# Kernel optimization log

Measured on AMD Instinct MI355X. Metric: run time of the kernel, lower is better.

The kernel has to match this reference:

```python
import jax, jax.numpy as jnp
import numpy as np

B, S, H, NH = 2, 2048, 1024, 16
HD = H // NH  # 64


def setup_inputs() -> dict:
    key = jax.random.key(0)
    ks = jax.random.split(key, 9)
    w = lambda k: jax.random.normal(k, (H, H), dtype=jnp.float32) * 0.02  # torch Linear weight [out,in]
    b = lambda k: jax.random.normal(k, (H,), dtype=jnp.float32) * 0.02
    return {
        "hidden_states": jax.random.normal(ks[0], (B, S, H), dtype=jnp.float32),
        "Wq": w(ks[1]), "bq": b(ks[2]),
        "Wk": w(ks[3]), "bk": b(ks[4]),
        "Wv": w(ks[5]), "bv": b(ks[6]),
        "Wo": w(ks[7]), "bo": b(ks[8]),
    }


def reference(hidden_states, Wq, bq, Wk, bk, Wv, bv, Wo, bo):
    b, s, h = hidden_states.shape
    nh, hd = NH, h // NH

    def proj(W, bias):
        y = hidden_states @ W.T + bias  # torch Linear: x W^T + b
        return y.reshape(b, s, nh, hd).transpose(0, 2, 1, 3)  # [b, h, s, d]

    q = proj(Wq, bq)
    k = proj(Wk, bk)
    v = proj(Wv, bv)

    scale = jnp.sqrt(jnp.asarray(hd, dtype=q.dtype))
    scores = jnp.einsum("bhqd,bhkd->bhqk", q, k) / scale  # [b, h, s, s]
    pos = jnp.arange(s)
    causal = pos[:, None] < pos[None, :]  # True where masked (key after query)
    scores = jnp.where(causal[None, None], -jnp.inf, scores)
    attn = jax.nn.softmax(scores, axis=-1)
    out = jnp.einsum("bhqk,bhkd->bhqd", attn, v)
    out = out.transpose(0, 2, 1, 3).reshape(b, s, h)
    return out @ Wo.T + bo
```

## Files before the change

kernel.cpp:

```cpp
#include <hip/hip_runtime.h>
#include <stdint.h>

typedef __bf16 bf16;
typedef __attribute__((ext_vector_type(2))) __bf16 bf16x2;
typedef __attribute__((ext_vector_type(4))) __bf16 bf16x4;
typedef __attribute__((ext_vector_type(8))) __bf16 bf16x8;
typedef __attribute__((ext_vector_type(4))) float f32x4;
typedef __attribute__((ext_vector_type(4))) short s16x4;

#define B_  2
#define S_  2048
#define H_  1024
#define NH_ 16
#define HD_ 64

__device__ __forceinline__ void glds16(const bf16* g, bf16* l) {
  __builtin_amdgcn_global_load_lds(
      (const __attribute__((address_space(1))) uint32_t*)g,
      (__attribute__((address_space(3))) uint32_t*)l, 16, 0, 0);
}

__device__ __forceinline__ f32x4 pv_mfma(bf16x4 a, bf16x4 b, f32x4 c) {
#if __has_builtin(__builtin_amdgcn_mfma_f32_16x16x16bf16_1k)
  union U { bf16x4 h; s16x4 s; };
  U ua; ua.h = a;
  U ub; ub.h = b;
  return __builtin_amdgcn_mfma_f32_16x16x16bf16_1k(ua.s, ub.s, c, 0, 0, 0);
#else
  f32x4 d;
  asm volatile("v_mfma_f32_16x16x16_bf16 %0, %1, %2, %3\n\ts_nop 7\n\ts_nop 7"
               : "=v"(d) : "v"(a), "v"(b), "v"(c));
  return d;
#endif
}

__device__ __forceinline__ void cvt16_store(const float4 v[4], bf16* dst) {
  bf16x8 o0, o1;
  o0[0] = (bf16)v[0].x; o0[1] = (bf16)v[0].y; o0[2] = (bf16)v[0].z; o0[3] = (bf16)v[0].w;
  o0[4] = (bf16)v[1].x; o0[5] = (bf16)v[1].y; o0[6] = (bf16)v[1].z; o0[7] = (bf16)v[1].w;
  o1[0] = (bf16)v[2].x; o1[1] = (bf16)v[2].y; o1[2] = (bf16)v[2].z; o1[3] = (bf16)v[2].w;
  o1[4] = (bf16)v[3].x; o1[5] = (bf16)v[3].y; o1[6] = (bf16)v[3].z; o1[7] = (bf16)v[3].w;
  *(bf16x8*)(dst)     = o0;
  *(bf16x8*)(dst + 8) = o1;
}

#define LD4(dst, src)                                                       \
  { dst[0] = *(const float4*)(src);      dst[1] = *(const float4*)((src) + 4); \
    dst[2] = *(const float4*)((src) + 8); dst[3] = *(const float4*)((src) + 12); }

__global__ __launch_bounds__(256) void gemm_qkv_f32(
    const float* __restrict__ X,
    const float* __restrict__ Wqf, const float* __restrict__ Wkf,
    const float* __restrict__ Wvf,
    const float* __restrict__ bq, const float* __restrict__ bk,
    const float* __restrict__ bv,
    bf16* __restrict__ Yq, bf16* __restrict__ Yk, bf16* __restrict__ Yv,
    float qscl)
{
  __shared__ __align__(16) bf16 As[2][128 * 32];
  __shared__ __align__(16) bf16 Bs[2][128 * 32];

  const int tid  = threadIdx.x;
  const int lane = tid & 63;
  const int wave = tid >> 6;

  const int m0  = blockIdx.y * 128;
  const int n0g = blockIdx.x * 128;
  const int seg = n0g >> 10;
  const float* W    = seg == 0 ? Wqf : (seg == 1 ? Wkf : Wvf);
  const float* bias = seg == 0 ? bq  : (seg == 1 ? bk  : bv);
  bf16*        Y    = seg == 0 ? Yq  : (seg == 1 ? Yk  : Yv);
  const float  ysc  = seg == 0 ? qscl : 1.0f;
  const int    n0   = n0g & 1023;

  const int wm = (wave >> 1) * 64;
  const int wn = (wave & 1) * 64;

  const int sr = tid >> 1, sc = (tid & 1) * 16;
  const float* Xs = X + (size_t)(m0 + sr) * 1024 + sc;
  const float* Ws = W + (size_t)(n0 + sr) * 1024 + sc;
  const int sdst = sr * 32 + sc;

  f32x4 acc[4][4] = {};
  float4 va[4], vb[4];

  LD4(va, Xs); LD4(vb, Ws);
  cvt16_store(va, &As[0][sdst]);
  cvt16_store(vb, &Bs[0][sdst]);

  int pb = 0;
  for (int k0 = 0; k0 < 1024; k0 += 32, pb ^= 1) {
    __syncthreads();
    const bool pre = k0 + 32 < 1024;
    if (pre) { LD4(va, Xs + k0 + 32); LD4(vb, Ws + k0 + 32); }

    bf16x8 a[4], b[4];
#pragma unroll
    for (int i = 0; i < 4; ++i)
      a[i] = *(const bf16x8*)&As[pb][(wm + i * 16 + (lane & 15)) * 32 + (lane >> 4) * 8];
#pragma unroll
    for (int i = 0; i < 4; ++i)
      b[i] = *(const bf16x8*)&Bs[pb][(wn + i * 16 + (lane & 15)) * 32 + (lane >> 4) * 8];
#pragma unroll
    for (int mi = 0; mi < 4; ++mi)
#pragma unroll
      for (int ni = 0; ni < 4; ++ni)
        acc[mi][ni] = __builtin_amdgcn_mfma_f32_16x16x32_bf16(a[mi], b[ni], acc[mi][ni], 0, 0, 0);

    if (pre) {
      cvt16_store(va, &As[pb ^ 1][sdst]);
      cvt16_store(vb, &Bs[pb ^ 1][sdst]);
    }
  }

#pragma unroll
  for (int mi = 0; mi < 4; ++mi) {
    const int row = m0 + wm + mi * 16 + (lane >> 4) * 4;
#pragma unroll
    for (int ni = 0; ni < 4; ++ni) {
      const int col = n0 + wn + ni * 16 + (lane & 15);
      const float bvv = bias[col];
#pragma unroll
      for (int r = 0; r < 4; ++r)
        Y[(size_t)(row + r) * 1024 + col] = (bf16)((acc[mi][ni][r] + bvv) * ysc);
    }
  }
}

__global__ __launch_bounds__(256) void gemm_o_f32w(
    const bf16* __restrict__ X, const float* __restrict__ W,
    const float* __restrict__ bias, float* __restrict__ Y)
{
  __shared__ __align__(16) bf16 As[2][128 * 32];
  __shared__ __align__(16) bf16 Bs[2][128 * 32];

  const int tid  = threadIdx.x;
  const int lane = tid & 63;
  const int wave = tid >> 6;
  const int m0 = blockIdx.y * 128;
  const int n0 = blockIdx.x * 128;
  const int wm = (wave >> 1) * 64;
  const int wn = (wave & 1) * 64;

  const int r0 = tid >> 2,            c0 = (tid & 3) * 8;
  const int r1 = (256 + tid) >> 2,    c1 = ((256 + tid) & 3) * 8;
  const int cb0 = (wave * 64) * 8;
  const int cb1 = (256 + wave * 64) * 8;

  const int sr = tid >> 1, sc = (tid & 1) * 16;
  const float* Ws = W + (size_t)(n0 + sr) * 1024 + sc;
  const int sdst = sr * 32 + sc;

  f32x4 acc[4][4] = {};
  float4 vb[4];

  glds16(X + (size_t)(m0 + r0) * 1024 + c0, &As[0][cb0]);
  glds16(X + (size_t)(m0 + r1) * 1024 + c1, &As[0][cb1]);
  LD4(vb, Ws);
  cvt16_store(vb, &Bs[0][sdst]);

  int pb = 0;
  for (int k0 = 0; k0 < 1024; k0 += 32, pb ^= 1) {
    __syncthreads();
    const bool pre = k0 + 32 < 1024;
    if (pre) {
      const int kn = k0 + 32;
      glds16(X + (size_t)(m0 + r0) * 1024 + kn + c0, &As[pb ^ 1][cb0]);
      glds16(X + (size_t)(m0 + r1) * 1024 + kn + c1, &As[pb ^ 1][cb1]);
      LD4(vb, Ws + kn);
    }

    bf16x8 a[4], b[4];
#pragma unroll
    for (int i = 0; i < 4; ++i)
      a[i] = *(const bf16x8*)&As[pb][(wm + i * 16 + (lane & 15)) * 32 + (lane >> 4) * 8];
#pragma unroll
    for (int i = 0; i < 4; ++i)
      b[i] = *(const bf16x8*)&Bs[pb][(wn + i * 16 + (lane & 15)) * 32 + (lane >> 4) * 8];
#pragma unroll
    for (int mi = 0; mi < 4; ++mi)
#pragma unroll
      for (int ni = 0; ni < 4; ++ni)
        acc[mi][ni] = __builtin_amdgcn_mfma_f32_16x16x32_bf16(a[mi], b[ni], acc[mi][ni], 0, 0, 0);

    if (pre) cvt16_store(vb, &Bs[pb ^ 1][sdst]);
  }

#pragma unroll
  for (int mi = 0; mi < 4; ++mi) {
    const int row = m0 + wm + mi * 16 + (lane >> 4) * 4;
#pragma unroll
    for (int ni = 0; ni < 4; ++ni) {
      const int col = n0 + wn + ni * 16 + (lane & 15);
      const float bvv = bias[col];
#pragma unroll
      for (int r = 0; r < 4; ++r)
        Y[(size_t)(row + r) * 1024 + col] = acc[mi][ni][r] + bvv;
    }
  }
}

__device__ __forceinline__ void attn_tile_step(
    const bf16* Ksb, const bf16* Vtb, const bf16x8 bq[2], int qrow, int k0,
    bool maskit, float& mr, float& lr, f32x4 oacc[4], int l15, int quad)
{
  f32x4 sacc[8] = {};
  __builtin_amdgcn_s_setprio(1);
#pragma unroll
  for (int ks = 0; ks < 2; ++ks) {
#pragma unroll
    for (int mb = 0; mb < 8; ++mb) {
      const int row = mb * 16 + l15;
      const int ch  = (ks * 4 + quad) ^ (l15 & 7);
      bf16x8 ak = *(const bf16x8*)&Ksb[row * 64 + ch * 8];
      sacc[mb] = __builtin_amdgcn_mfma_f32_16x16x32_bf16(ak, bq[ks], sacc[mb], 0, 0, 0);
    }
  }
  __builtin_amdgcn_s_setprio(0);

  if (maskit) {
#pragma unroll
    for (int mb = 0; mb < 8; ++mb) {
      const int kb = k0 + mb * 16 + quad * 4;
#pragma unroll
      for (int r = 0; r < 4; ++r)
        if (kb + r > qrow) sacc[mb][r] = -1e30f;
    }
  }

  float mx = -1e30f;
#pragma unroll
  for (int mb = 0; mb < 8; ++mb)
    mx = fmaxf(mx, fmaxf(fmaxf(sacc[mb][0], sacc[mb][1]),
                         fmaxf(sacc[mb][2], sacc[mb][3])));
  mx = fmaxf(mx, __shfl_xor(mx, 16, 64));
  mx = fmaxf(mx, __shfl_xor(mx, 32, 64));

  float sum = 0.0f;
  bf16x4 pwv[8];
#pragma unroll
  for (int mb = 0; mb < 8; ++mb) {
    bf16x4 pw;
#pragma unroll
    for (int r = 0; r < 4; ++r) {
      const float p = __builtin_amdgcn_exp2f(sacc[mb][r] - mr);
      sum += p;
      pw[r] = (bf16)p;
    }
    pwv[mb] = pw;
  }
  sum += __shfl_xor(sum, 16, 64);
  sum += __shfl_xor(sum, 32, 64);

  __builtin_amdgcn_s_setprio(1);
#pragma unroll
  for (int mb = 0; mb < 8; ++mb) {
#pragma unroll
    for (int db = 0; db < 4; ++db) {
      const int vch = ((mb * 4 + quad) ^ (l15 & 7)) * 4;
      bf16x4 av = *(const bf16x4*)&Vtb[(db * 16 + l15) * 128 + vch];
      oacc[db] = pv_mfma(av, pwv[mb], oacc[db]);
    }
  }
  __builtin_amdgcn_s_setprio(0);

  lr += sum;
  if (!__all(mx <= mr + 8.0f)) {
    const float mnew  = fmaxf(mr, mx);
    const float alpha = __builtin_amdgcn_exp2f(mr - mnew);
    lr *= alpha;
#pragma unroll
    for (int db = 0; db < 4; ++db)
#pragma unroll
      for (int r = 0; r < 4; ++r) oacc[db][r] *= alpha;
    mr = mnew;
  }
}

__global__ __launch_bounds__(256, 2) void attn_causal(
    const bf16* __restrict__ Q, const bf16* __restrict__ K,
    const bf16* __restrict__ V, bf16* __restrict__ O)
{
  const int lin  = blockIdx.x;
  const int slot = lin >> 3;
  const int bh   = (lin & 7) * 4 + (slot >> 4);
  const int pair = slot & 15;
  const int b    = bh >> 4;
  const int h    = bh & 15;

  const int tid  = threadIdx.x;
  const int lane = tid & 63;
  const int wave = tid >> 6;
  const int quad = lane >> 4;
  const int l15  = lane & 15;
  const size_t headoff = (size_t)b * S_ * H_ + (size_t)h * HD_;
  const bf16* Kp = K + headoff;
  const bf16* Vp = V + headoff;

  __shared__ __align__(16) bf16 Ks[2][128 * 64];
  __shared__ __align__(16) bf16 Vt[2][64 * 128];

  const int qlo = pair, qhi = 31 - pair;
  const int nl  = (qlo >> 1) + 1;
  const int nh  = (qhi >> 1) + 1;
  const int qrowL = qlo * 64 + wave * 16 + l15;
  const int qrowH = qhi * 64 + wave * 16 + l15;

  bf16x8 bqL[2], bqH[2];
  bqL[0] = *(const bf16x8*)(Q + headoff + (size_t)qrowL * H_ + quad * 8);
  bqL[1] = *(const bf16x8*)(Q + headoff + (size_t)qrowL * H_ + 32 + quad * 8);
  bqH[0] = *(const bf16x8*)(Q + headoff + (size_t)qrowH * H_ + quad * 8);
  bqH[1] = *(const bf16x8*)(Q + headoff + (size_t)qrowH * H_ + 32 + quad * 8);

  const int vr = lane * 2;
  const int vc = wave * 16;

#define STAGE_K(k0_, buf_)                                                  \
  {                                                                         \
    _Pragma("unroll")                                                       \
    for (int i = 0; i < 4; ++i) {                                           \
      const int n = i * 256 + tid;                                          \
      const int row = n >> 3;                                               \
      const int cg  = (n & 7) ^ (row & 7);                                  \
      glds16(Kp + (size_t)((k0_) + row) * H_ + cg * 8,                      \
             &Ks[buf_][(i * 256 + wave * 64) * 8]);                         \
    }                                                                       \
  }

#define LOAD_V(k0_)                                                         \
  {                                                                         \
    vreg[0] = *(const bf16x8*)(Vp + (size_t)((k0_) + vr) * H_ + vc);        \
    vreg[1] = *(const bf16x8*)(Vp + (size_t)((k0_) + vr) * H_ + vc + 8);    \
    vreg[2] = *(const bf16x8*)(Vp + (size_t)((k0_) + vr + 1) * H_ + vc);    \
    vreg[3] = *(const bf16x8*)(Vp + (size_t)((k0_) + vr + 1) * H_ + vc + 8);\
  }

#define WRITE_V(buf_)                                                       \
  {                                                                         \
    _Pragma("unroll")                                                       \
    for (int e = 0; e < 8; ++e) {                                           \
      const int sw = (((vr >> 2) ^ e) * 4) + (vr & 3);                      \
      bf16x2 p0; p0[0] = vreg[0][e]; p0[1] = vreg[2][e];                    \
      *(bf16x2*)&Vt[buf_][(vc + e) * 128 + sw] = p0;                        \
      bf16x2 p1; p1[0] = vreg[1][e]; p1[1] = vreg[3][e];                    \
      *(bf16x2*)&Vt[buf_][(vc + 8 + e) * 128 + sw] = p1;                    \
    }                                                                       \
  }

  bf16x8 vreg[4];

  STAGE_K(0, 0);
  LOAD_V(0);
  WRITE_V(0);
  __syncthreads();

  float mrL = 0.0f, lrL = 0.0f, mrH = 0.0f, lrH = 0.0f;
  f32x4 oL[4] = {}, oH[4] = {};

  for (int it = 0; it < nh; ++it) {
    const int c = it & 1;
    const bool pre = (it + 1 < nh);

    if (pre) {
      STAGE_K((it + 1) * 128, c ^ 1);
      LOAD_V((it + 1) * 128);
    }

    attn_tile_step(Ks[c], Vt[c], bqH, qrowH, it * 128, it == nh - 1,
                   mrH, lrH, oH, l15, quad);
    if (it < nl)
      attn_tile_step(Ks[c], Vt[c], bqL, qrowL, it * 128, it == nl - 1,
                     mrL, lrL, oL, l15, quad);

    if (pre) {
      WRITE_V(c ^ 1);
      __syncthreads();
    }
  }

  const float invL = 1.0f / lrL;
#pragma unroll
  for (int db = 0; db < 4; ++db) {
    bf16x4 o;
#pragma unroll
    for (int r = 0; r < 4; ++r) o[r] = (bf16)(oL[db][r] * invL);
    *(bf16x4*)(O + headoff + (size_t)qrowL * H_ + db * 16 + quad * 4) = o;
  }
  const float invH = 1.0f / lrH;
#pragma unroll
  for (int db = 0; db < 4; ++db) {
    bf16x4 o;
#pragma unroll
    for (int r = 0; r < 4; ++r) o[r] = (bf16)(oH[db][r] * invH);
    *(bf16x4*)(O + headoff + (size_t)qrowH * H_ + db * 16 + quad * 4) = o;
  }
#undef STAGE_K
#undef LOAD_V
#undef WRITE_V
}

extern "C" void kernel_launch(void* const* d_in, const int* in_sizes, int n_in,
                              void* d_out, int out_size, void* d_ws, size_t ws_size,
                              hipStream_t stream) {
  const float* hs = (const float*)d_in[0];
  const float* Wq = (const float*)d_in[1]; const float* bq = (const float*)d_in[2];
  const float* Wk = (const float*)d_in[3]; const float* bk = (const float*)d_in[4];
  const float* Wv = (const float*)d_in[5]; const float* bv = (const float*)d_in[6];
  const float* Wo = (const float*)d_in[7]; const float* bo = (const float*)d_in[8];
  float* out = (float*)d_out;

  const size_t elems = (size_t)B_ * S_ * H_;
  bf16* Qw = (bf16*)d_ws;
  bf16* Kw = Qw + elems;
  bf16* Vw = Kw + elems;
  bf16* AO = Vw + elems;

  const float QSCL = 0.125f * 1.44269504f;

  gemm_qkv_f32<<<dim3(24, 32), dim3(256), 0, stream>>>(
      hs, Wq, Wk, Wv, bq, bk, bv, Qw, Kw, Vw, QSCL);

  attn_causal<<<dim3(512), dim3(256), 0, stream>>>(Qw, Kw, Vw, AO);

  gemm_o_f32w<<<dim3(8, 32), dim3(256), 0, stream>>>(AO, Wo, bo, out);
}
```

Measured before the change: 247.5 us.

## Remap GEMM blocks per XCD and coalesce fp32 tile loads

Both projection GEMMs move to a 1-D grid whose block index is remapped so that each XCD (blockIdx mod 8) handles a contiguous band of 4 M-tiles across all N-tiles. The aim is better L2 reuse of the activation rows inside each XCD. The fp32 staging loads are also reorganized so four consecutive threads cover one 32-float row segment, giving more coalesced global reads, and the LDS store becomes a contiguous tid*8 write. The remap depends on the hardware dispatching blocks round-robin across XCDs.

```diff
diff --git a/kernel.cpp b/kernel.cpp
--- a/kernel.cpp
+++ b/kernel.cpp
@@ -34,19 +34,12 @@
 #endif
 }
 
-__device__ __forceinline__ void cvt16_store(const float4 v[4], bf16* dst) {
-  bf16x8 o0, o1;
-  o0[0] = (bf16)v[0].x; o0[1] = (bf16)v[0].y; o0[2] = (bf16)v[0].z; o0[3] = (bf16)v[0].w;
-  o0[4] = (bf16)v[1].x; o0[5] = (bf16)v[1].y; o0[6] = (bf16)v[1].z; o0[7] = (bf16)v[1].w;
-  o1[0] = (bf16)v[2].x; o1[1] = (bf16)v[2].y; o1[2] = (bf16)v[2].z; o1[3] = (bf16)v[2].w;
-  o1[4] = (bf16)v[3].x; o1[5] = (bf16)v[3].y; o1[6] = (bf16)v[3].z; o1[7] = (bf16)v[3].w;
-  *(bf16x8*)(dst)     = o0;
-  *(bf16x8*)(dst + 8) = o1;
-}
-
-#define LD4(dst, src)                                                       \
-  { dst[0] = *(const float4*)(src);      dst[1] = *(const float4*)((src) + 4); \
-    dst[2] = *(const float4*)((src) + 8); dst[3] = *(const float4*)((src) + 12); }
+__device__ __forceinline__ bf16x8 cvt8(const float4 a, const float4 b) {
+  bf16x8 o;
+  o[0] = (bf16)a.x; o[1] = (bf16)a.y; o[2] = (bf16)a.z; o[3] = (bf16)a.w;
+  o[4] = (bf16)b.x; o[5] = (bf16)b.y; o[6] = (bf16)b.z; o[7] = (bf16)b.w;
+  return o;
+}
 
 __global__ __launch_bounds__(256) void gemm_qkv_f32(
     const float* __restrict__ X,
@@ -64,8 +57,13 @@
   const int lane = tid & 63;
   const int wave = tid >> 6;
 
-  const int m0  = blockIdx.y * 128;
-  const int n0g = blockIdx.x * 128;
+  const int f   = blockIdx.x;
+  const int xcd = f & 7;
+  const int i   = f >> 3;
+  const int bx  = i % 24;
+  const int by  = xcd * 4 + i / 24;
+  const int m0  = by * 128;
+  const int n0g = bx * 128;
   const int seg = n0g >> 10;
   const float* W    = seg == 0 ? Wqf : (seg == 1 ? Wkf : Wvf);
   const float* bias = seg == 0 ? bq  : (seg == 1 ? bk  : bv);
@@ -76,41 +74,50 @@
   const int wm = (wave >> 1) * 64;
   const int wn = (wave & 1) * 64;
 
-  const int sr = tid >> 1, sc = (tid & 1) * 16;
-  const float* Xs = X + (size_t)(m0 + sr) * 1024 + sc;
-  const float* Ws = W + (size_t)(n0 + sr) * 1024 + sc;
-  const int sdst = sr * 32 + sc;
+  const int r0 = tid >> 2, q0 = (tid & 3) * 8;
+  const int r1 = r0 + 64;
+  const float* Xa0 = X + (size_t)(m0 + r0) * 1024 + q0;
+  const float* Xa1 = X + (size_t)(m0 + r1) * 1024 + q0;
+  const float* Wb0 = W + (size_t)(n0 + r0) * 1024 + q0;
+  const float* Wb1 = W + (size_t)(n0 + r1) * 1024 + q0;
 
   f32x4 acc[4][4] = {};
   float4 va[4], vb[4];
 
-  LD4(va, Xs); LD4(vb, Ws);
-  cvt16_store(va, &As[0][sdst]);
-  cvt16_store(vb, &Bs[0][sdst]);
+#define LDT(k)                                                              \
+  { va[0] = *(const float4*)(Xa0 + (k));  va[1] = *(const float4*)(Xa0 + (k) + 4); \
+    va[2] = *(const float4*)(Xa1 + (k));  va[3] = *(const float4*)(Xa1 + (k) + 4); \
+    vb[0] = *(const float4*)(Wb0 + (k));  vb[1] = *(const float4*)(Wb0 + (k) + 4); \
+    vb[2] = *(const float4*)(Wb1 + (k));  vb[3] = *(const float4*)(Wb1 + (k) + 4); }
+#define STT(buf)                                                            \
+  { *(bf16x8*)&As[buf][tid * 8]         = cvt8(va[0], va[1]);               \
+    *(bf16x8*)&As[buf][(tid + 256) * 8] = cvt8(va[2], va[3]);               \
+    *(bf16x8*)&Bs[buf][tid * 8]         = cvt8(vb[0], vb[1]);               \
+    *(bf16x8*)&Bs[buf][(tid + 256) * 8] = cvt8(vb[2], vb[3]); }
+
+  LDT(0);
+  STT(0);
 
   int pb = 0;
   for (int k0 = 0; k0 < 1024; k0 += 32, pb ^= 1) {
     __syncthreads();
     const bool pre = k0 + 32 < 1024;
-    if (pre) { LD4(va, Xs + k0 + 32); LD4(vb, Ws + k0 + 32); }
+    if (pre) LDT(k0 + 32);
 
     bf16x8 a[4], b[4];
 #pragma unroll
-    for (int i = 0; i < 4; ++i)
-      a[i] = *(const bf16x8*)&As[pb][(wm + i * 16 + (lane & 15)) * 32 + (lane >> 4) * 8];
-#pragma unroll
-    for (int i = 0; i < 4; ++i)
-      b[i] = *(const bf16x8*)&Bs[pb][(wn + i * 16 + (lane & 15)) * 32 + (lane >> 4) * 8];
+    for (int j = 0; j < 4; ++j)
+      a[j] = *(const bf16x8*)&As[pb][(wm + j * 16 + (lane & 15)) * 32 + (lane >> 4) * 8];
+#pragma unroll
+    for (int j = 0; j < 4; ++j)
+      b[j] = *(const bf16x8*)&Bs[pb][(wn + j * 16 + (lane & 15)) * 32 + (lane >> 4) * 8];
 #pragma unroll
     for (int mi = 0; mi < 4; ++mi)
 #pragma unroll
       for (int ni = 0; ni < 4; ++ni)
         acc[mi][ni] = __builtin_amdgcn_mfma_f32_16x16x32_bf16(a[mi], b[ni], acc[mi][ni], 0, 0, 0);
 
-    if (pre) {
-      cvt16_store(va, &As[pb ^ 1][sdst]);
-      cvt16_store(vb, &Bs[pb ^ 1][sdst]);
-    }
+    if (pre) STT(pb ^ 1);
   }
 
 #pragma unroll
@@ -125,6 +132,8 @@
         Y[(size_t)(row + r) * 1024 + col] = (bf16)((acc[mi][ni][r] + bvv) * ysc);
     }
   }
+#undef LDT
+#undef STT
 }
 
 __global__ __launch_bounds__(256) void gemm_o_f32w(
@@ -137,27 +146,42 @@
   const int tid  = threadIdx.x;
   const int lane = tid & 63;
   const int wave = tid >> 6;
-  const int m0 = blockIdx.y * 128;
-  const int n0 = blockIdx.x * 128;
+
+  const int f   = blockIdx.x;
+  const int xcd = f & 7;
+  const int i   = f >> 3;
+  const int bx  = i % 8;
+  const int by  = xcd * 4 + i / 8;
+  const int m0  = by * 128;
+  const int n0  = bx * 128;
+
   const int wm = (wave >> 1) * 64;
   const int wn = (wave & 1) * 64;
 
-  const int r0 = tid >> 2,            c0 = (tid & 3) * 8;
-  const int r1 = (256 + tid) >> 2,    c1 = ((256 + tid) & 3) * 8;
+  const int ar0 = tid >> 2,           ac0 = (tid & 3) * 8;
+  const int ar1 = (256 + tid) >> 2,   ac1 = ((256 + tid) & 3) * 8;
   const int cb0 = (wave * 64) * 8;
   const int cb1 = (256 + wave * 64) * 8;
 
-  const int sr = tid >> 1, sc = (tid & 1) * 16;
-  const float* Ws = W + (size_t)(n0 + sr) * 1024 + sc;
-  const int sdst = sr * 32 + sc;
+  const int r0 = tid >> 2, q0 = (tid & 3) * 8;
+  const int r1 = r0 + 64;
+  const float* Wb0 = W + (size_t)(n0 + r0) * 1024 + q0;
+  const float* Wb1 = W + (size_t)(n0 + r1) * 1024 + q0;
 
   f32x4 acc[4][4] = {};
   float4 vb[4];
 
-  glds16(X + (size_t)(m0 + r0) * 1024 + c0, &As[0][cb0]);
-  glds16(X + (size_t)(m0 + r1) * 1024 + c1, &As[0][cb1]);
-  LD4(vb, Ws);
-  cvt16_store(vb, &Bs[0][sdst]);
+#define LDB(k)                                                              \
+  { vb[0] = *(const float4*)(Wb0 + (k));  vb[1] = *(const float4*)(Wb0 + (k) + 4); \
+    vb[2] = *(const float4*)(Wb1 + (k));  vb[3] = *(const float4*)(Wb1 + (k) + 4); }
+#define STB(buf)                                                            \
+  { *(bf16x8*)&Bs[buf][tid * 8]         = cvt8(vb[0], vb[1]);               \
+    *(bf16x8*)&Bs[buf][(tid + 256) * 8] = cvt8(vb[2], vb[3]); }
+
+  glds16(X + (size_t)(m0 + ar0) * 1024 + ac0, &As[0][cb0]);
+  glds16(X + (size_t)(m0 + ar1) * 1024 + ac1, &As[0][cb1]);
+  LDB(0);
+  STB(0);
 
   int pb = 0;
   for (int k0 = 0; k0 < 1024; k0 += 32, pb ^= 1) {
@@ -165,25 +189,25 @@
     const bool pre = k0 + 32 < 1024;
     if (pre) {
       const int kn = k0 + 32;
-      glds16(X + (size_t)(m0 + r0) * 1024 + kn + c0, &As[pb ^ 1][cb0]);
-      glds16(X + (size_t)(m0 + r1) * 1024 + kn + c1, &As[pb ^ 1][cb1]);
-      LD4(vb, Ws + kn);
+      glds16(X + (size_t)(m0 + ar0) * 1024 + kn + ac0, &As[pb ^ 1][cb0]);
+      glds16(X + (size_t)(m0 + ar1) * 1024 + kn + ac1, &As[pb ^ 1][cb1]);
+      LDB(kn);
     }
 
     bf16x8 a[4], b[4];
 #pragma unroll
-    for (int i = 0; i < 4; ++i)
-      a[i] = *(const bf16x8*)&As[pb][(wm + i * 16 + (lane & 15)) * 32 + (lane >> 4) * 8];
-#pragma unroll
-    for (int i = 0; i < 4; ++i)
-      b[i] = *(const bf16x8*)&Bs[pb][(wn + i * 16 + (lane & 15)) * 32 + (lane >> 4) * 8];
+    for (int j = 0; j < 4; ++j)
+      a[j] = *(const bf16x8*)&As[pb][(wm + j * 16 + (lane & 15)) * 32 + (lane >> 4) * 8];
+#pragma unroll
+    for (int j = 0; j < 4; ++j)
+      b[j] = *(const bf16x8*)&Bs[pb][(wn + j * 16 + (lane & 15)) * 32 + (lane >> 4) * 8];
 #pragma unroll
     for (int mi = 0; mi < 4; ++mi)
 #pragma unroll
       for (int ni = 0; ni < 4; ++ni)
         acc[mi][ni] = __builtin_amdgcn_mfma_f32_16x16x32_bf16(a[mi], b[ni], acc[mi][ni], 0, 0, 0);
 
-    if (pre) cvt16_store(vb, &Bs[pb ^ 1][sdst]);
+    if (pre) STB(pb ^ 1);
   }
 
 #pragma unroll
@@ -198,6 +222,8 @@
         Y[(size_t)(row + r) * 1024 + col] = acc[mi][ni][r] + bvv;
     }
   }
+#undef LDB
+#undef STB
 }
 
 __device__ __forceinline__ void attn_tile_step(
@@ -318,12 +344,12 @@
 #define STAGE_K(k0_, buf_)                                                  \
   {                                                                         \
     _Pragma("unroll")                                                       \
-    for (int i = 0; i < 4; ++i) {                                           \
-      const int n = i * 256 + tid;                                          \
+    for (int j = 0; j < 4; ++j) {                                           \
+      const int n = j * 256 + tid;                                          \
       const int row = n >> 3;                                               \
       const int cg  = (n & 7) ^ (row & 7);                                  \
       glds16(Kp + (size_t)((k0_) + row) * H_ + cg * 8,                      \
-             &Ks[buf_][(i * 256 + wave * 64) * 8]);                         \
+             &Ks[buf_][(j * 256 + wave * 64) * 8]);                         \
     }                                                                       \
   }
 
@@ -417,10 +443,10 @@
 
   const float QSCL = 0.125f * 1.44269504f;
 
-  gemm_qkv_f32<<<dim3(24, 32), dim3(256), 0, stream>>>(
+  gemm_qkv_f32<<<dim3(768), dim3(256), 0, stream>>>(
       hs, Wq, Wk, Wv, bq, bk, bv, Qw, Kw, Vw, QSCL);
 
   attn_causal<<<dim3(512), dim3(256), 0, stream>>>(Qw, Kw, Vw, AO);
 
-  gemm_o_f32w<<<dim3(8, 32), dim3(256), 0, stream>>>(AO, Wo, bo, out);
-}
+  gemm_o_f32w<<<dim3(256), dim3(256), 0, stream>>>(AO, Wo, bo, out);
+}
```

Measured after the change: 219.3 us. 11.4% less time.
